# Kernel tuning notes

Hardware: AMD Instinct MI355X
Metric: run time of the kernel (lower is better)

The kernel has to match this reference:

```python
import jax, jax.numpy as jnp
import numpy as np

NUM_HEADS = 16
WINDOW = 512
EPS = 1e-5


def layer_norm(x, g, b):
    m = jnp.mean(x, axis=-1, keepdims=True)
    v = jnp.var(x, axis=-1, keepdims=True)
    return (x - m) * jax.lax.rsqrt(v + EPS) * g + b


def rope(x, pos):
    # x: [B,H,S,D], rotate-half RoPE with base 10000
    D = x.shape[-1]
    inv_freq = 1.0 / (10000.0 ** (jnp.arange(0, D, 2, dtype=jnp.float32) / D))
    ang = pos[:, None].astype(jnp.float32) * inv_freq  # [S, D/2]
    cos = jnp.concatenate([jnp.cos(ang), jnp.cos(ang)], axis=-1)
    sin = jnp.concatenate([jnp.sin(ang), jnp.sin(ang)], axis=-1)
    x1, x2 = jnp.split(x, 2, axis=-1)
    rot = jnp.concatenate([-x2, x1], axis=-1)
    return x * cos + rot * sin


def setup_inputs() -> dict:
    key = jax.random.key(0)
    ks = jax.random.split(key, 8)
    B, S, Dm = 2, 2048, 1024
    Dff = 4 * Dm
    sc = 0.02
    return {
        'hidden_states': jax.random.normal(ks[0], (B, S, Dm), jnp.float32),
        'ln1_g': jnp.ones((Dm,), jnp.float32),
        'ln1_b': jnp.zeros((Dm,), jnp.float32),
        'wq': jax.random.normal(ks[1], (Dm, Dm), jnp.float32) * sc,
        'bq': jnp.zeros((Dm,), jnp.float32),
        'wk': jax.random.normal(ks[2], (Dm, Dm), jnp.float32) * sc,
        'bk': jnp.zeros((Dm,), jnp.float32),
        'wv': jax.random.normal(ks[3], (Dm, Dm), jnp.float32) * sc,
        'bv': jnp.zeros((Dm,), jnp.float32),
        'wo': jax.random.normal(ks[4], (Dm, Dm), jnp.float32) * sc,
        'bo': jnp.zeros((Dm,), jnp.float32),
        'ln2_g': jnp.ones((Dm,), jnp.float32),
        'ln2_b': jnp.zeros((Dm,), jnp.float32),
        'w1': jax.random.normal(ks[5], (Dm, Dff), jnp.float32) * sc,
        'b1': jnp.zeros((Dff,), jnp.float32),
        'w2': jax.random.normal(ks[6], (Dff, Dm), jnp.float32) * sc,
        'b2': jnp.zeros((Dm,), jnp.float32),
        'global_token_indices': jax.random.randint(ks[7], (8,), 0, S, jnp.int32),
    }


def reference(hidden_states, ln1_g, ln1_b, wq, bq, wk, bk, wv, bv, wo, bo,
              ln2_g, ln2_b, w1, b1, w2, b2, global_token_indices):
    B, S, Dm = hidden_states.shape
    H = NUM_HEADS
    Dh = Dm // H

    # --- attention block ---
    x = layer_norm(hidden_states, ln1_g, ln1_b)
    heads = lambda t: t.reshape(B, S, H, Dh).transpose(0, 2, 1, 3)  # [B,H,S,Dh]
    q = heads(x @ wq + bq)
    k = heads(x @ wk + bk)
    v = heads(x @ wv + bv)

    pos = jnp.arange(S)
    q = rope(q, pos)
    k = rope(k, pos)

    scores = jnp.einsum('bhqd,bhkd->bhqk', q, k) / jnp.sqrt(jnp.float32(Dh))
    i = pos[:, None]
    j = pos[None, :]
    causal = j <= i
    band = causal & ((i - j) < WINDOW)
    is_global = jnp.zeros((S,), bool).at[global_token_indices].set(True)
    allowed = band | (causal & (is_global[None, :] | is_global[:, None]))
    scores = jnp.where(allowed[None, None], scores, jnp.float32(-1e9))
    attn = jax.nn.softmax(scores, axis=-1)
    ctx = jnp.einsum('bhqk,bhkd->bhqd', attn, v)
    ctx = ctx.transpose(0, 2, 1, 3).reshape(B, S, Dm)
    attn_out = ctx @ wo + bo
    h = hidden_states + attn_out

    # --- MLP block ---
    y = layer_norm(h, ln2_g, ln2_b)
    mlp = jax.nn.gelu(y @ w1 + b1, approximate=False) @ w2 + b2
    return h + mlp
```

## Files before the change

### kernel.cpp

```cpp
#include <hip/hip_runtime.h>

typedef unsigned short u16;
typedef __bf16 bf16x8 __attribute__((ext_vector_type(8)));
typedef short s16x8 __attribute__((ext_vector_type(8)));
typedef float f32x4 __attribute__((ext_vector_type(4)));

#define NB 2
#define SS 2048
#define DM 1024
#define NH 16
#define DH 64
#define DFF 4096

__device__ __forceinline__ u16 f2bf(float f) {
    unsigned u = __float_as_uint(f);
    u += 0x7fff + ((u >> 16) & 1);
    return (u16)(u >> 16);
}
__device__ __forceinline__ float bf2f(u16 h) {
    return __uint_as_float(((unsigned)h) << 16);
}
__device__ __forceinline__ void gld_lds16(const void* g, void* l) {
    __builtin_amdgcn_global_load_lds(
        (const __attribute__((address_space(1))) unsigned int*)(size_t)g,
        (__attribute__((address_space(3))) unsigned int*)(unsigned)(size_t)l,
        16, 0, 0);
}
__device__ __forceinline__ float gelu_f(float x) {
    return 0.5f * x * (1.f + erff(x * 0.70710678118654752f));
}

__global__ void wtrans_kernel(const float* __restrict__ w, u16* __restrict__ wt,
                              int K, int N) {
    __shared__ unsigned tl[64][65];
    int n0 = blockIdx.x * 64, k0 = blockIdx.y * 64, t = threadIdx.x;
    for (int it = 0; it < 16; ++it) {
        int e = it * 256 + t; int r = e >> 6, c = e & 63;
        tl[r][c] = f2bf(w[(size_t)(k0 + r) * N + n0 + c]);
    }
    __syncthreads();
    for (int it = 0; it < 16; ++it) {
        int e = it * 256 + t; int r = e >> 6, c = e & 63;
        wt[(size_t)(n0 + r) * K + k0 + c] = (u16)tl[c][r];
    }
}

__global__ void wtrans4_kernel(const float* __restrict__ a, const float* __restrict__ b,
                               const float* __restrict__ c, const float* __restrict__ d,
                               u16* __restrict__ oa, u16* __restrict__ ob,
                               u16* __restrict__ oc, u16* __restrict__ od) {
    __shared__ unsigned tl[64][65];
    const float* w; u16* wt;
    switch (blockIdx.z) {
        case 0: w = a; wt = oa; break;
        case 1: w = b; wt = ob; break;
        case 2: w = c; wt = oc; break;
        default: w = d; wt = od; break;
    }
    int n0 = blockIdx.x * 64, k0 = blockIdx.y * 64, t = threadIdx.x;
    for (int it = 0; it < 16; ++it) {
        int e = it * 256 + t; int r = e >> 6, cc = e & 63;
        tl[r][cc] = f2bf(w[(size_t)(k0 + r) * DM + n0 + cc]);
    }
    __syncthreads();
    for (int it = 0; it < 16; ++it) {
        int e = it * 256 + t; int r = e >> 6, cc = e & 63;
        wt[(size_t)(n0 + r) * DM + k0 + cc] = (u16)tl[cc][r];
    }
}

__global__ void build_aux(const int* __restrict__ gti, unsigned long long* __restrict__ kmask,
                          const float* __restrict__ bq, const float* __restrict__ bk,
                          const float* __restrict__ bv, float* __restrict__ bias3) {
    int t = threadIdx.x;
    if (t < 32) {
        unsigned long long m = 0ull;
        #pragma unroll
        for (int i = 0; i < 8; ++i) {
            int g = gti[i];
            if ((g >> 6) == t) m |= 1ull << (g & 63);
        }
        kmask[t] = m;
    }
    for (int i = t; i < 1024; i += 256) {
        bias3[i] = bq[i]; bias3[1024 + i] = bk[i]; bias3[2048 + i] = bv[i];
    }
}

template <bool INIT>
__global__ __launch_bounds__(256) void ln_kernel(const float* __restrict__ x,
                                                 const float* __restrict__ g,
                                                 const float* __restrict__ b,
                                                 u16* __restrict__ out,
                                                 const float* __restrict__ ib,
                                                 float* __restrict__ iout) {
    int row = blockIdx.x, t = threadIdx.x;
    const float4 v = ((const float4*)(x + (size_t)row * DM))[t];
    float s  = v.x + v.y + v.z + v.w;
    float sq = v.x * v.x + v.y * v.y + v.z * v.z + v.w * v.w;
    #pragma unroll
    for (int m = 1; m < 64; m <<= 1) { s += __shfl_xor(s, m); sq += __shfl_xor(sq, m); }
    __shared__ float ss[4], ssq[4];
    int wv = t >> 6, lane = t & 63;
    if (lane == 0) { ss[wv] = s; ssq[wv] = sq; }
    __syncthreads();
    s  = ss[0] + ss[1] + ss[2] + ss[3];
    sq = ssq[0] + ssq[1] + ssq[2] + ssq[3];
    float mean = s * (1.f / DM);
    float var  = sq * (1.f / DM) - mean * mean;
    float rs   = rsqrtf(var + 1e-5f);
    float4 gg = ((const float4*)g)[t];
    float4 bb = ((const float4*)b)[t];
    ushort4 o;
    o.x = f2bf((v.x - mean) * rs * gg.x + bb.x);
    o.y = f2bf((v.y - mean) * rs * gg.y + bb.y);
    o.z = f2bf((v.z - mean) * rs * gg.z + bb.z);
    o.w = f2bf((v.w - mean) * rs * gg.w + bb.w);
    ((ushort4*)(out + (size_t)row * DM))[t] = o;
    if (INIT) {
        float4 b2 = ((const float4*)ib)[t];
        float4 iv; iv.x = v.x + b2.x; iv.y = v.y + b2.y; iv.z = v.z + b2.z; iv.w = v.w + b2.w;
        ((float4*)(iout + (size_t)row * DM))[t] = iv;
    }
}

__global__ __launch_bounds__(256) void rope_kernel(const u16* __restrict__ qkv,
                                                   u16* __restrict__ qh,
                                                   u16* __restrict__ kh) {
    int idx = blockIdx.x * 256 + threadIdx.x;
    int d = idx & 31;
    int s = (idx >> 5) & (SS - 1);
    int h = (idx >> 16) & (NH - 1);
    int b = idx >> 20;
    size_t src = ((size_t)(b * SS + s)) * 3072 + h * DH + d;
    size_t dst = ((size_t)((b * NH + h) * SS + s)) * DH + d;
    float inv = powf(10000.f, -(float)d * (1.f / 32.f));
    float ang = (float)s * inv;
    float sn, cs;
    sincosf(ang, &sn, &cs);
    const float QSC = 0.125f;
    float x1 = bf2f(qkv[src]), x2 = bf2f(qkv[src + 32]);
    qh[dst]      = f2bf((x1 * cs - x2 * sn) * QSC);
    qh[dst + 32] = f2bf((x2 * cs + x1 * sn) * QSC);
    x1 = bf2f(qkv[src + 1024]); x2 = bf2f(qkv[src + 1024 + 32]);
    kh[dst]      = f2bf(x1 * cs - x2 * sn);
    kh[dst + 32] = f2bf(x2 * cs + x1 * sn);
}

__global__ __launch_bounds__(256) void vtrans_kernel(const u16* __restrict__ qkv,
                                                     u16* __restrict__ vt) {
    __shared__ unsigned tile[64][65];
    int st = blockIdx.x, bh = blockIdx.y;
    int b = bh >> 4, h = bh & 15, t = threadIdx.x;
    const u16* src = qkv + ((size_t)b * SS + st * 64) * 3072 + 2048 + h * DH;
    for (int it = 0; it < 16; ++it) {
        int e = it * 256 + t; int r = e >> 6, c = e & 63;
        tile[r][c] = src[(size_t)r * 3072 + c];
    }
    __syncthreads();
    u16* dst = vt + ((size_t)bh * DH) * SS + st * 64;
    for (int it = 0; it < 16; ++it) {
        int e = it * 256 + t; int d = e >> 6, s = e & 63;
        dst[(size_t)d * SS + s] = (u16)tile[s][d];
    }
}

template <int MODE>
__global__ __launch_bounds__(256) void gemm_bt(const u16* __restrict__ A,
                                               const u16* __restrict__ Bt,
                                               const float* __restrict__ bias,
                                               const float* __restrict__ res,
                                               void* __restrict__ Cout,
                                               int M, int N, int K, int ldk) {
    const int bm = blockIdx.y * 128, bn = blockIdx.x * 128;
    const int koff = blockIdx.z * K;
    const int t = threadIdx.x, wv = t >> 6, lane = t & 63;
    const int lr = lane & 15, lq = lane >> 4;
    const int wm = (wv >> 1) * 64, wn = (wv & 1) * 64;
    __shared__ __align__(16) u16 As[2][128 * 64];
    __shared__ __align__(16) u16 Bs[2][128 * 64];
    f32x4 acc[4][4] = {};

    auto stage = [&](int kb, int buf) {
        #pragma unroll
        for (int p = 0; p < 4; ++p) {
            int c = p * 256 + t;
            int r = c >> 3;
            int gc = ((c & 7) ^ (r & 7)) * 8;
            gld_lds16(A + (size_t)(bm + r) * ldk + kb + gc,
                      As[buf] + (size_t)(p * 256 + wv * 64) * 8);
            gld_lds16(Bt + (size_t)(bn + r) * ldk + kb + gc,
                      Bs[buf] + (size_t)(p * 256 + wv * 64) * 8);
        }
    };

    stage(koff, 0);
    int pb = 0;
    for (int k0 = 0; k0 < K; k0 += 64) {
        __syncthreads();
        if (k0 + 64 < K) stage(koff + k0 + 64, pb ^ 1);
        const u16* Ac = As[pb];
        const u16* Bc = Bs[pb];
        #pragma unroll
        for (int ks = 0; ks < 2; ++ks) {
            bf16x8 af[4], bfr[4];
            #pragma unroll
            for (int mi = 0; mi < 4; ++mi) {
                int row = wm + mi * 16 + lr;
                af[mi] = *(const bf16x8*)&Ac[row * 64 + (((ks * 4 + lq) ^ (row & 7)) * 8)];
            }
            #pragma unroll
            for (int ni = 0; ni < 4; ++ni) {
                int row = wn + ni * 16 + lr;
                bfr[ni] = *(const bf16x8*)&Bc[row * 64 + (((ks * 4 + lq) ^ (row & 7)) * 8)];
            }
            #pragma unroll
            for (int mi = 0; mi < 4; ++mi)
                #pragma unroll
                for (int ni = 0; ni < 4; ++ni)
                    acc[mi][ni] = __builtin_amdgcn_mfma_f32_16x16x32_bf16(af[mi], bfr[ni], acc[mi][ni], 0, 0, 0);
        }
        pb ^= 1;
    }
    #pragma unroll
    for (int mi = 0; mi < 4; ++mi) {
        int row0 = bm + wm + mi * 16 + lq * 4;
        #pragma unroll
        for (int ni = 0; ni < 4; ++ni) {
            int col = bn + wn + ni * 16 + lr;
            float bv = (MODE == 3) ? 0.f : bias[col];
            #pragma unroll
            for (int r = 0; r < 4; ++r) {
                float v = acc[mi][ni][r] + bv;
                size_t off = (size_t)(row0 + r) * N + col;
                if (MODE == 1) v += res[off];
                if (MODE == 2) v = gelu_f(v);
                if (MODE == 0 || MODE == 2) ((u16*)Cout)[off] = f2bf(v);
                else if (MODE == 1)         ((float*)Cout)[off] = v;
                else                        atomicAdd((float*)Cout + off, v);
            }
        }
    }
}

__global__ __launch_bounds__(256) void attn_kernel(const u16* __restrict__ qh,
                                                   const u16* __restrict__ kh,
                                                   const u16* __restrict__ vt,
                                                   const unsigned long long* __restrict__ kmask,
                                                   u16* __restrict__ ctx) {
    const int qt = blockIdx.x, bh = blockIdx.y;
    const int b = bh >> 4, h = bh & 15;
    const int t = threadIdx.x, wv = t >> 6, lane = t & 63;
    const int lr = lane & 15, lq = lane >> 4;
    const int q0 = qt * 64;

    __shared__ __align__(16) u16 Qs[64 * 64];
    __shared__ __align__(16) u16 Ks[2][64 * 64];
    __shared__ __align__(16) u16 Vs[2][64 * 64];
    __shared__ __align__(16) u16 Ps[64 * 64];

    const u16* qbase = qh + ((size_t)bh * SS) * DH;
    const u16* kbase = kh + ((size_t)bh * SS) * DH;
    const u16* vbase = vt + ((size_t)bh * DH) * SS;

    #pragma unroll
    for (int p = 0; p < 2; ++p) {
        int c = p * 256 + t; int r = c >> 3, sl = c & 7;
        gld_lds16(qbase + (size_t)(q0 + r) * DH + ((sl ^ (r & 7)) * 8),
                  Qs + (size_t)(p * 256 + wv * 64) * 8);
    }

    float sum_part[4] = {0.f, 0.f, 0.f, 0.f};
    f32x4 acc_o[4] = {};

    const int lim = qt - 8;
    int cur = 0;
    while (cur < lim && kmask[cur] == 0ull) ++cur;
    {
        int k0 = cur * 64;
        #pragma unroll
        for (int p = 0; p < 2; ++p) {
            int c = p * 256 + t; int r = c >> 3; int gc = ((c & 7) ^ (r & 7)) * 8;
            gld_lds16(kbase + (size_t)(k0 + r) * DH + gc, Ks[0] + (size_t)(p * 256 + wv * 64) * 8);
            gld_lds16(vbase + (size_t)r * SS + k0 + gc,  Vs[0] + (size_t)(p * 256 + wv * 64) * 8);
        }
    }
    int pb = 0;
    while (cur >= 0) {
        int nxt = cur + 1;
        while (nxt < lim && kmask[nxt] == 0ull) ++nxt;
        if (nxt > qt) nxt = -1;
        __syncthreads();
        if (nxt >= 0) {
            int k0n = nxt * 64;
            #pragma unroll
            for (int p = 0; p < 2; ++p) {
                int c = p * 256 + t; int r = c >> 3; int gc = ((c & 7) ^ (r & 7)) * 8;
                gld_lds16(kbase + (size_t)(k0n + r) * DH + gc, Ks[pb ^ 1] + (size_t)(p * 256 + wv * 64) * 8);
                gld_lds16(vbase + (size_t)r * SS + k0n + gc,  Vs[pb ^ 1] + (size_t)(p * 256 + wv * 64) * 8);
            }
        }
        const u16* Kt = Ks[pb];
        const u16* Vt = Vs[pb];
        const int k0 = cur * 64;

        f32x4 s_acc[4] = {};
        #pragma unroll
        for (int ks = 0; ks < 2; ++ks) {
            const int arow = wv * 16 + lr;
            bf16x8 af = *(const bf16x8*)&Qs[arow * 64 + (((ks * 4 + lq) ^ (arow & 7)) * 8)];
            #pragma unroll
            for (int ni = 0; ni < 4; ++ni) {
                const int brow = ni * 16 + lr;
                bf16x8 bfr = *(const bf16x8*)&Kt[brow * 64 + (((ks * 4 + lq) ^ (brow & 7)) * 8)];
                s_acc[ni] = __builtin_amdgcn_mfma_f32_16x16x32_bf16(af, bfr, s_acc[ni], 0, 0, 0);
            }
        }
        float sv[4][4];
        if (cur >= qt - 7 && cur != qt) {
            #pragma unroll
            for (int ni = 0; ni < 4; ++ni)
                #pragma unroll
                for (int r = 0; r < 4; ++r) sv[ni][r] = __expf(s_acc[ni][r]);
        } else if (cur == qt) {
            #pragma unroll
            for (int ni = 0; ni < 4; ++ni) {
                int j = ni * 16 + lr;
                #pragma unroll
                for (int r = 0; r < 4; ++r) {
                    int i = wv * 16 + lq * 4 + r;
                    float p = __expf(s_acc[ni][r]);
                    sv[ni][r] = (j <= i) ? p : 0.f;
                }
            }
        } else {
            unsigned long long cm = kmask[cur];
            #pragma unroll
            for (int ni = 0; ni < 4; ++ni) {
                int j = k0 + ni * 16 + lr;
                bool gj = (cm >> (ni * 16 + lr)) & 1ull;
                #pragma unroll
                for (int r = 0; r < 4; ++r) {
                    int i = q0 + wv * 16 + lq * 4 + r;
                    bool ok = ((i - j) < 512) | gj;
                    float p = __expf(s_acc[ni][r]);
                    sv[ni][r] = ok ? p : 0.f;
                }
            }
        }
        #pragma unroll
        for (int ni = 0; ni < 4; ++ni) {
            int col = ni * 16 + lr;
            #pragma unroll
            for (int r = 0; r < 4; ++r) {
                int row = wv * 16 + lq * 4 + r;
                sum_part[r] += sv[ni][r];
                Ps[row * 64 + (((col >> 3) ^ (row & 7)) * 8) + (col & 7)] = f2bf(sv[ni][r]);
            }
        }
        #pragma unroll
        for (int ks = 0; ks < 2; ++ks) {
            const int arow = wv * 16 + lr;
            bf16x8 af = *(const bf16x8*)&Ps[arow * 64 + (((ks * 4 + lq) ^ (arow & 7)) * 8)];
            #pragma unroll
            for (int ni = 0; ni < 4; ++ni) {
                const int brow = ni * 16 + lr;
                bf16x8 bfr = *(const bf16x8*)&Vt[brow * 64 + (((ks * 4 + lq) ^ (brow & 7)) * 8)];
                acc_o[ni] = __builtin_amdgcn_mfma_f32_16x16x32_bf16(af, bfr, acc_o[ni], 0, 0, 0);
            }
        }
        cur = nxt; pb ^= 1;
    }
    float inv_l[4];
    #pragma unroll
    for (int r = 0; r < 4; ++r) {
        float ls = sum_part[r];
        #pragma unroll
        for (int m = 1; m < 16; m <<= 1) ls += __shfl_xor(ls, m, 16);
        inv_l[r] = 1.f / ls;
    }
    u16* obase = ctx + ((size_t)b * SS) * DM + h * DH;
    #pragma unroll
    for (int ni = 0; ni < 4; ++ni)
        #pragma unroll
        for (int r = 0; r < 4; ++r) {
            int i = q0 + wv * 16 + lq * 4 + r;
            obase[(size_t)i * DM + ni * 16 + lr] = f2bf(acc_o[ni][r] * inv_l[r]);
        }
}

__global__ __launch_bounds__(256) void attn_fix_kernel(const u16* __restrict__ qh,
                                                       const u16* __restrict__ kh,
                                                       const u16* __restrict__ qkv,
                                                       const int* __restrict__ gti,
                                                       u16* __restrict__ ctx) {
    const int gidx = blockIdx.x, bh = blockIdx.y;
    const int b = bh >> 4, h = bh & 15;
    const int t = threadIdx.x, wv = t >> 6, lane = t & 63;
    const int i = gti[gidx];

    __shared__ float qsh[64];
    if (t < 64) qsh[t] = bf2f(qh[((size_t)bh * SS + i) * DH + t]);
    __syncthreads();
    float qreg[64];
    #pragma unroll
    for (int c = 0; c < 16; ++c) {
        float4 qv = ((const float4*)qsh)[c];
        qreg[c * 4 + 0] = qv.x; qreg[c * 4 + 1] = qv.y;
        qreg[c * 4 + 2] = qv.z; qreg[c * 4 + 3] = qv.w;
    }

    const u16* kb = kh + (size_t)bh * SS * DH;
    const u16* vb = qkv + (size_t)b * SS * 3072 + 2048 + h * DH;

    float Oacc[64];
    #pragma unroll
    for (int d = 0; d < 64; ++d) Oacc[d] = 0.f;
    float lacc = 0.f;

    for (int j0 = wv * 64; j0 <= i; j0 += 256) {
        const int j = j0 + lane;
        const bool valid = (j <= i);
        const int jc = valid ? j : i;
        const s16x8* krow = (const s16x8*)(kb + (size_t)jc * DH);
        float part[8];
        #pragma unroll
        for (int c = 0; c < 8; ++c) {
            s16x8 kv = krow[c];
            float p0 = 0.f;
            #pragma unroll
            for (int e = 0; e < 8; ++e) p0 += qreg[c * 8 + e] * bf2f((u16)kv[e]);
            part[c] = p0;
        }
        float s = ((part[0] + part[1]) + (part[2] + part[3])) +
                  ((part[4] + part[5]) + (part[6] + part[7]));
        const float p = valid ? __expf(s) : 0.f;
        lacc += p;
        const s16x8* vrow = (const s16x8*)(vb + (size_t)jc * 3072);
        #pragma unroll
        for (int c = 0; c < 8; ++c) {
            s16x8 vv = vrow[c];
            #pragma unroll
            for (int e = 0; e < 8; ++e) Oacc[c * 8 + e] += p * bf2f((u16)vv[e]);
        }
    }
    #pragma unroll
    for (int m = 1; m < 64; m <<= 1) {
        lacc += __shfl_xor(lacc, m);
        #pragma unroll
        for (int d = 0; d < 64; ++d) Oacc[d] += __shfl_xor(Oacc[d], m);
    }
    float out = 0.f;
    #pragma unroll
    for (int d = 0; d < 64; ++d) out = (lane == d) ? Oacc[d] : out;
    __shared__ float osum[4][64];
    __shared__ float lsum[4];
    osum[wv][lane] = out;
    if (lane == 0) lsum[wv] = lacc;
    __syncthreads();
    if (wv == 0) {
        float ot = osum[0][lane] + osum[1][lane] + osum[2][lane] + osum[3][lane];
        float lt = lsum[0] + lsum[1] + lsum[2] + lsum[3];
        ctx[((size_t)b * SS + i) * DM + h * DH + lane] = f2bf(ot / lt);
    }
}

extern "C" void kernel_launch(void* const* d_in, const int* in_sizes, int n_in,
                              void* d_out, int out_size, void* d_ws, size_t ws_size,
                              hipStream_t stream) {
    (void)in_sizes; (void)n_in; (void)out_size; (void)ws_size;
    const float* hidden = (const float*)d_in[0];
    const float* ln1_g  = (const float*)d_in[1];
    const float* ln1_b  = (const float*)d_in[2];
    const float* wq = (const float*)d_in[3];  const float* bq = (const float*)d_in[4];
    const float* wk = (const float*)d_in[5];  const float* bk = (const float*)d_in[6];
    const float* wv = (const float*)d_in[7];  const float* bv = (const float*)d_in[8];
    const float* wo = (const float*)d_in[9];  const float* bo = (const float*)d_in[10];
    const float* ln2_g = (const float*)d_in[11];
    const float* ln2_b = (const float*)d_in[12];
    const float* w1 = (const float*)d_in[13]; const float* b1 = (const float*)d_in[14];
    const float* w2 = (const float*)d_in[15]; const float* b2 = (const float*)d_in[16];
    const int*  gti = (const int*)d_in[17];

    char* ws = (char*)d_ws;
    const size_t MB = 1u << 20;
    u16* wqt  = (u16*)(ws + 0 * MB);
    u16* wkt  = (u16*)(ws + 2 * MB);
    u16* wvt  = (u16*)(ws + 4 * MB);
    u16* wot  = (u16*)(ws + 6 * MB);
    u16* w1t  = (u16*)(ws + 8 * MB);
    u16* w2t  = (u16*)(ws + 16 * MB);
    u16* xb   = (u16*)(ws + 24 * MB);
    u16* ctx  = xb;
    u16* qkv  = (u16*)(ws + 32 * MB);
    u16* qhb  = (u16*)(ws + 56 * MB);
    u16* khb  = (u16*)(ws + 64 * MB);
    u16* vtb  = (u16*)(ws + 72 * MB);
    float* hb = (float*)(ws + 80 * MB);
    u16* act  = (u16*)(ws + 32 * MB);
    u16* yb   = (u16*)(ws + 64 * MB);
    unsigned long long* kmask = (unsigned long long*)(ws + 96 * MB);
    float* bias3 = (float*)(ws + 96 * MB + 8192);

    wtrans4_kernel<<<dim3(16, 16, 4), 256, 0, stream>>>(wq, wk, wv, wo, wqt, wkt, wvt, wot);
    wtrans_kernel<<<dim3(64, 16), 256, 0, stream>>>(w1, w1t, DM, DFF);
    wtrans_kernel<<<dim3(16, 64), 256, 0, stream>>>(w2, w2t, DFF, DM);
    build_aux<<<1, 256, 0, stream>>>(gti, kmask, bq, bk, bv, bias3);

    ln_kernel<false><<<NB * SS, 256, 0, stream>>>(hidden, ln1_g, ln1_b, xb, nullptr, nullptr);

    gemm_bt<0><<<dim3(24, 32), 256, 0, stream>>>(xb, wqt, bias3, nullptr, qkv, NB * SS, 3072, DM, DM);

    rope_kernel<<<(NB * NH * SS * 32) / 256, 256, 0, stream>>>(qkv, qhb, khb);
    vtrans_kernel<<<dim3(SS / 64, NB * NH), 256, 0, stream>>>(qkv, vtb);

    attn_kernel<<<dim3(SS / 64, NB * NH), 256, 0, stream>>>(qhb, khb, vtb, kmask, ctx);
    attn_fix_kernel<<<dim3(8, NB * NH), 256, 0, stream>>>(qhb, khb, qkv, gti, ctx);

    gemm_bt<1><<<dim3(8, 32), 256, 0, stream>>>(ctx, wot, bo, hidden, hb, NB * SS, DM, DM, DM);
    ln_kernel<true><<<NB * SS, 256, 0, stream>>>(hb, ln2_g, ln2_b, yb, b2, (float*)d_out);
    gemm_bt<2><<<dim3(32, 32), 256, 0, stream>>>(yb, w1t, b1, nullptr, act, NB * SS, DFF, DM, DM);
    gemm_bt<3><<<dim3(8, 32, 2), 256, 0, stream>>>(act, w2t, nullptr, nullptr, d_out, NB * SS, DM, DFF / 2, DFF);
}
```

Before: 392.3 us.

## Add 256x256-tile 512-thread GEMM with 4-stage LDS pipeline for QKV and MLP

Adds a new GEMM kernel that uses 256x256 output tiles, 8 waves, a 4-buffer swizzled LDS ring filled by direct global-to-LDS loads, and explicit waitcnt/barrier scheduling. It replaces the QKV projection and both MLP GEMMs with this kernel, and the down-projection now splits K four ways with atomics. The aim is more data reuse per tile and better latency hiding. In exchange it uses large LDS and register footprints, launches far fewer blocks (e.g. 192 for QKV, 256 for the MLP up-projection), and adds more atomic traffic.

After: 419.5 us. 1.07x slower.

```diff
diff --git a/kernel.cpp b/kernel.cpp
--- a/kernel.cpp
+++ b/kernel.cpp
@@ -243,6 +243,97 @@
     }
 }
 
+template <int MODE>
+__global__ __launch_bounds__(512, 2) void gemm256(const u16* __restrict__ A,
+                                                  const u16* __restrict__ Bt,
+                                                  const float* __restrict__ bias,
+                                                  void* __restrict__ Cout,
+                                                  int M, int N, int K, int ldk) {
+    const int bm = blockIdx.y * 256, bn = blockIdx.x * 256;
+    const int koff = blockIdx.z * K;
+    const int t = threadIdx.x, wv = t >> 6, lane = t & 63;
+    const int lr = lane & 15, lq = lane >> 4;
+    const int wm = (wv >> 2) * 128, wn = (wv & 3) * 64;
+    __shared__ __align__(16) u16 As[4 * 256 * 32];
+    __shared__ __align__(16) u16 Bs[4 * 256 * 32];
+    f32x4 acc[8][4] = {};
+
+    auto stage = [&](int st) {
+        const int buf = st & 3;
+        const int kb = koff + st * 32;
+        #pragma unroll
+        for (int p = 0; p < 2; ++p) {
+            int c = p * 512 + t;
+            int r = c >> 2, sl = c & 3;
+            int gc = (sl ^ ((r >> 1) & 3)) * 8;
+            gld_lds16(A + (size_t)(bm + r) * ldk + kb + gc,
+                      As + (size_t)buf * 8192 + (size_t)(p * 512 + wv * 64) * 8);
+            gld_lds16(Bt + (size_t)(bn + r) * ldk + kb + gc,
+                      Bs + (size_t)buf * 8192 + (size_t)(p * 512 + wv * 64) * 8);
+        }
+    };
+
+    auto compute = [&](int s) {
+        const u16* Ac = As + (size_t)(s & 3) * 8192;
+        const u16* Bc = Bs + (size_t)(s & 3) * 8192;
+        bf16x8 af[8], bfv[4];
+        #pragma unroll
+        for (int mi = 0; mi < 8; ++mi) {
+            int row = wm + mi * 16 + lr;
+            af[mi] = *(const bf16x8*)&Ac[row * 32 + ((lq ^ ((row >> 1) & 3)) * 8)];
+        }
+        #pragma unroll
+        for (int ni = 0; ni < 4; ++ni) {
+            int row = wn + ni * 16 + lr;
+            bfv[ni] = *(const bf16x8*)&Bc[row * 32 + ((lq ^ ((row >> 1) & 3)) * 8)];
+        }
+        __builtin_amdgcn_s_setprio(1);
+        #pragma unroll
+        for (int mi = 0; mi < 8; ++mi)
+            #pragma unroll
+            for (int ni = 0; ni < 4; ++ni)
+                acc[mi][ni] = __builtin_amdgcn_mfma_f32_16x16x32_bf16(af[mi], bfv[ni], acc[mi][ni], 0, 0, 0);
+        __builtin_amdgcn_s_setprio(0);
+    };
+
+    const int NS = K >> 5;
+    stage(0);
+    stage(1);
+    for (int s = 0; s < NS - 2; ++s) {
+        stage(s + 2);
+        asm volatile("s_waitcnt vmcnt(8) lgkmcnt(0)" ::: "memory");
+        __builtin_amdgcn_s_barrier();
+        asm volatile("" ::: "memory");
+        compute(s);
+    }
+    asm volatile("s_waitcnt vmcnt(4) lgkmcnt(0)" ::: "memory");
+    __builtin_amdgcn_s_barrier();
+    asm volatile("" ::: "memory");
+    compute(NS - 2);
+    asm volatile("s_waitcnt vmcnt(0) lgkmcnt(0)" ::: "memory");
+    __builtin_amdgcn_s_barrier();
+    asm volatile("" ::: "memory");
+    compute(NS - 1);
+
+    #pragma unroll
+    for (int mi = 0; mi < 8; ++mi) {
+        int row0 = bm + wm + mi * 16 + lq * 4;
+        #pragma unroll
+        for (int ni = 0; ni < 4; ++ni) {
+            int col = bn + wn + ni * 16 + lr;
+            float bv = (MODE == 3) ? 0.f : bias[col];
+            #pragma unroll
+            for (int r = 0; r < 4; ++r) {
+                float v = acc[mi][ni][r] + bv;
+                size_t off = (size_t)(row0 + r) * N + col;
+                if (MODE == 2) v = gelu_f(v);
+                if (MODE == 0 || MODE == 2) ((u16*)Cout)[off] = f2bf(v);
+                else                        atomicAdd((float*)Cout + off, v);
+            }
+        }
+    }
+}
+
 __global__ __launch_bounds__(256) void attn_kernel(const u16* __restrict__ qh,
                                                    const u16* __restrict__ kh,
                                                    const u16* __restrict__ vt,
@@ -509,7 +600,8 @@
 
     ln_kernel<false><<<NB * SS, 256, 0, stream>>>(hidden, ln1_g, ln1_b, xb, nullptr, nullptr);
 
-    gemm_bt<0><<<dim3(24, 32), 256, 0, stream>>>(xb, wqt, bias3, nullptr, qkv, NB * SS, 3072, DM, DM);
+    gemm256<0><<<dim3(3072 / 256, (NB * SS) / 256), 512, 0, stream>>>(
+        xb, wqt, bias3, qkv, NB * SS, 3072, DM, DM);
 
     rope_kernel<<<(NB * NH * SS * 32) / 256, 256, 0, stream>>>(qkv, qhb, khb);
     vtrans_kernel<<<dim3(SS / 64, NB * NH), 256, 0, stream>>>(qkv, vtb);
@@ -519,6 +611,8 @@
 
     gemm_bt<1><<<dim3(8, 32), 256, 0, stream>>>(ctx, wot, bo, hidden, hb, NB * SS, DM, DM, DM);
     ln_kernel<true><<<NB * SS, 256, 0, stream>>>(hb, ln2_g, ln2_b, yb, b2, (float*)d_out);
-    gemm_bt<2><<<dim3(32, 32), 256, 0, stream>>>(yb, w1t, b1, nullptr, act, NB * SS, DFF, DM, DM);
-    gemm_bt<3><<<dim3(8, 32, 2), 256, 0, stream>>>(act, w2t, nullptr, nullptr, d_out, NB * SS, DM, DFF / 2, DFF);
-}
+    gemm256<2><<<dim3(DFF / 256, (NB * SS) / 256), 512, 0, stream>>>(
+        yb, w1t, b1, act, NB * SS, DFF, DM, DM);
+    gemm256<3><<<dim3(DM / 256, (NB * SS) / 256, 4), 512, 0, stream>>>(
+        act, w2t, nullptr, d_out, NB * SS, DM, DFF / 4, DFF);
+}
```
